# Performance work log

Hardware: AMD Instinct MI355X
Metric: run time of the kernel (lower is better)

Reference implementation:

```python
import jax, jax.numpy as jnp
import numpy as np

N_BEST = 50          # hypotheses per utterance segment
NUM_SEG = 1_000_000  # number of utterance segments
TOTAL = N_BEST * NUM_SEG


def setup_inputs() -> dict:
    key = jax.random.key(0)
    scores = jax.random.normal(key, (TOTAL,), dtype=jnp.float32)
    # per-segment n-best counts; sum(nBestIndex) == len(scores)
    nBestIndex = jnp.full((NUM_SEG,), N_BEST, dtype=jnp.int32)
    return {"scores": scores, "nBestIndex": nBestIndex}


def reference(scores, nBestIndex):
    # Segmented (ragged) softmax: softmax within each contiguous n-best group.
    # Equivalent to the torch loop with log_score=False, fused into one pass.
    num_seg = nBestIndex.shape[0]
    total = scores.shape[0]
    # segment id for each score element
    seg = jnp.repeat(jnp.arange(num_seg, dtype=jnp.int32), nBestIndex,
                     total_repeat_length=total)
    # numerically stable segmented softmax
    seg_max = jax.ops.segment_max(scores, seg, num_segments=num_seg)
    exps = jnp.exp(scores - seg_max[seg])
    seg_sum = jax.ops.segment_sum(exps, seg, num_segments=num_seg)
    return exps / seg_sum[seg]
```

## Files before the change

kernel.cpp:

```cpp
#include <hip/hip_runtime.h>
#include <math.h>


#define GSEG   16
#define SPG    4
#define SBLOCK 256
#define SEGS_B ((SBLOCK / GSEG) * SPG)

__global__ __launch_bounds__(256) void scan_local_kernel(
    const int* __restrict__ counts, int n_seg,
    int* __restrict__ local_scan, int* __restrict__ block_sums) {
    __shared__ int sm[256];
    const int t = threadIdx.x;
    const int g = blockIdx.x * 256 + t;
    const int v = (g < n_seg) ? counts[g] : 0;
    sm[t] = v;
    __syncthreads();
    for (int off = 1; off < 256; off <<= 1) {
        int y = (t >= off) ? sm[t - off] : 0;
        __syncthreads();
        sm[t] += y;
        __syncthreads();
    }
    if (g < n_seg) local_scan[g] = sm[t] - v;
    if (t == 255) block_sums[blockIdx.x] = sm[255];
}

__global__ __launch_bounds__(256) void scan_bsums_kernel(
    int* __restrict__ bsum, int nb) {
    __shared__ int sm[256];
    const int t = threadIdx.x;
    const int per = (nb + 255) >> 8;
    const int beg = t * per;
    const int end = (beg + per < nb) ? beg + per : nb;
    int tot = 0;
    for (int j = beg; j < end; ++j) tot += bsum[j];
    sm[t] = tot;
    __syncthreads();
    for (int off = 1; off < 256; off <<= 1) {
        int y = (t >= off) ? sm[t - off] : 0;
        __syncthreads();
        sm[t] += y;
        __syncthreads();
    }
    int run = sm[t] - tot;
    for (int j = beg; j < end; ++j) {
        int v = bsum[j];
        bsum[j] = run;
        run += v;
    }
}

__global__ __launch_bounds__(SBLOCK) void seg_softmax_kernel(
    const float* __restrict__ scores,
    const int* __restrict__ local_scan, const int* __restrict__ bsum,
    float* __restrict__ out, int n_seg, int total) {
    __shared__ int starts[SEGS_B + 1];

    const int tid  = threadIdx.x;
    const int seg0 = blockIdx.x * SEGS_B;

    if (tid <= SEGS_B) {
        const int s = seg0 + tid;
        starts[tid] = (s < n_seg) ? (local_scan[s] + bsum[s >> 8]) : total;
    }
    __syncthreads();

    const int p   = tid & (GSEG - 1);
    const int grp = tid >> 4;

    int st[SPG], c[SPG];
    #pragma unroll
    for (int q = 0; q < SPG; ++q) {
        const int ls = grp * SPG + q;
        st[q] = starts[ls];
        c[q]  = starts[ls + 1] - st[q];
    }

    bool all_small = true;
    #pragma unroll
    for (int q = 0; q < SPG; ++q) all_small &= (c[q] <= 4 * GSEG);

    if (all_small) {
        float v[SPG][4];
        #pragma unroll
        for (int q = 0; q < SPG; ++q) {
            #pragma unroll
            for (int r = 0; r < 4; ++r) {
                const int idx = p + r * GSEG;
                v[q][r] = (idx < c[q]) ? scores[st[q] + idx] : -INFINITY;
            }
        }

        #pragma unroll
        for (int q = 0; q < SPG; ++q) {
            if (c[q] <= 0) continue;
            float m = fmaxf(fmaxf(v[q][0], v[q][1]), fmaxf(v[q][2], v[q][3]));
            #pragma unroll
            for (int off = 1; off < GSEG; off <<= 1)
                m = fmaxf(m, __shfl_xor(m, off, GSEG));

            const float e0 = __expf(v[q][0] - m);
            const float e1 = __expf(v[q][1] - m);
            const float e2 = __expf(v[q][2] - m);
            const float e3 = __expf(v[q][3] - m);
            float s = (e0 + e1) + (e2 + e3);
            #pragma unroll
            for (int off = 1; off < GSEG; off <<= 1)
                s += __shfl_xor(s, off, GSEG);

            const float inv = __builtin_amdgcn_rcpf(s);
            if (p < c[q])             out[st[q] + p]            = e0 * inv;
            if (p + GSEG < c[q])      out[st[q] + p + GSEG]     = e1 * inv;
            if (p + 2 * GSEG < c[q])  out[st[q] + p + 2 * GSEG] = e2 * inv;
            if (p + 3 * GSEG < c[q])  out[st[q] + p + 3 * GSEG] = e3 * inv;
        }
    } else {
        #pragma unroll
        for (int q = 0; q < SPG; ++q) {
            if (c[q] <= 0) continue;
            float m = -INFINITY;
            for (int j = p; j < c[q]; j += GSEG)
                m = fmaxf(m, scores[st[q] + j]);
            #pragma unroll
            for (int off = 1; off < GSEG; off <<= 1)
                m = fmaxf(m, __shfl_xor(m, off, GSEG));

            float s = 0.0f;
            for (int j = p; j < c[q]; j += GSEG)
                s += __expf(scores[st[q] + j] - m);
            #pragma unroll
            for (int off = 1; off < GSEG; off <<= 1)
                s += __shfl_xor(s, off, GSEG);

            const float inv = __builtin_amdgcn_rcpf(s);
            for (int j = p; j < c[q]; j += GSEG)
                out[st[q] + j] = __expf(scores[st[q] + j] - m) * inv;
        }
    }
}

extern "C" void kernel_launch(void* const* d_in, const int* in_sizes, int n_in,
                              void* d_out, int out_size, void* d_ws, size_t ws_size,
                              hipStream_t stream) {
    const float* scores = (const float*)d_in[0];
    const int*   counts = (const int*)d_in[1];
    float* out = (float*)d_out;
    const int n_seg = in_sizes[1];
    const int total = in_sizes[0];

    int* local_scan = (int*)d_ws;
    const int nblocksA = (n_seg + 255) / 256;
    int* block_sums = local_scan + n_seg;

    scan_local_kernel<<<nblocksA, 256, 0, stream>>>(counts, n_seg, local_scan, block_sums);
    scan_bsums_kernel<<<1, 256, 0, stream>>>(block_sums, nblocksA);

    const int nblocksC = (n_seg + SEGS_B - 1) / SEGS_B;
    seg_softmax_kernel<<<nblocksC, SBLOCK, 0, stream>>>(
        scores, local_scan, block_sums, out, n_seg, total);
}
```

Baseline: 364.7 us.

## Stage each block's contiguous score span in LDS with float4 loads and stores

Each softmax block now copies its whole contiguous score range into shared memory with vectorized float4 global loads, computes the segmented softmax in LDS, and writes the results back with float4 stores. The aim is to replace scattered per-lane scalar global accesses with fully coalesced wide transfers. It adds a 13KB LDS buffer per block, which may limit occupancy, and extra barriers. A fallback path handles spans that are too large or misaligned.

```diff
diff --git a/kernel.cpp b/kernel.cpp
--- a/kernel.cpp
+++ b/kernel.cpp
@@ -6,6 +6,7 @@
 #define SPG    4
 #define SBLOCK 256
 #define SEGS_B ((SBLOCK / GSEG) * SPG)
+#define LDS_FLOATS 3328
 
 __global__ __launch_bounds__(256) void scan_local_kernel(
     const int* __restrict__ counts, int n_seg,
@@ -55,6 +56,7 @@
     const float* __restrict__ scores,
     const int* __restrict__ local_scan, const int* __restrict__ bsum,
     float* __restrict__ out, int n_seg, int total) {
+    __shared__ float sm[LDS_FLOATS];
     __shared__ int starts[SEGS_B + 1];
 
     const int tid  = threadIdx.x;
@@ -64,78 +66,115 @@
         const int s = seg0 + tid;
         starts[tid] = (s < n_seg) ? (local_scan[s] + bsum[s >> 8]) : total;
     }
-    __syncthreads();
-
-    const int p   = tid & (GSEG - 1);
-    const int grp = tid >> 4;
-
-    int st[SPG], c[SPG];
-    #pragma unroll
-    for (int q = 0; q < SPG; ++q) {
-        const int ls = grp * SPG + q;
-        st[q] = starts[ls];
-        c[q]  = starts[ls + 1] - st[q];
-    }
-
-    bool all_small = true;
-    #pragma unroll
-    for (int q = 0; q < SPG; ++q) all_small &= (c[q] <= 4 * GSEG);
-
-    if (all_small) {
-        float v[SPG][4];
+
+    const int base  = local_scan[seg0] + bsum[seg0 >> 8];
+    const int eseg  = seg0 + SEGS_B;
+    const int bend  = (eseg < n_seg) ? (local_scan[eseg] + bsum[eseg >> 8]) : total;
+    const int span  = bend - base;
+
+    if (span <= LDS_FLOATS && (base & 3) == 0) {
+        const float4* __restrict__ src = (const float4*)(scores + base);
+        const int nvec = span >> 2;
+        for (int i = tid; i < nvec; i += SBLOCK)
+            ((float4*)sm)[i] = src[i];
+        for (int i = (nvec << 2) + tid; i < span; i += SBLOCK)
+            sm[i] = scores[base + i];
+        __syncthreads();
+
+        const int p   = tid & (GSEG - 1);
+        const int grp = tid >> 4;
+
+        int st[SPG], c[SPG];
         #pragma unroll
         for (int q = 0; q < SPG; ++q) {
-            #pragma unroll
-            for (int r = 0; r < 4; ++r) {
-                const int idx = p + r * GSEG;
-                v[q][r] = (idx < c[q]) ? scores[st[q] + idx] : -INFINITY;
-            }
+            const int ls = grp * SPG + q;
+            st[q] = starts[ls] - base;
+            c[q]  = starts[ls + 1] - starts[ls];
         }
 
         #pragma unroll
         for (int q = 0; q < SPG; ++q) {
             if (c[q] <= 0) continue;
-            float m = fmaxf(fmaxf(v[q][0], v[q][1]), fmaxf(v[q][2], v[q][3]));
+            if (c[q] <= 4 * GSEG) {
+                float v0 = -INFINITY, v1 = -INFINITY, v2 = -INFINITY, v3 = -INFINITY;
+                const int i0 = p, i1 = p + GSEG, i2 = p + 2 * GSEG, i3 = p + 3 * GSEG;
+                if (i0 < c[q]) v0 = sm[st[q] + i0];
+                if (i1 < c[q]) v1 = sm[st[q] + i1];
+                if (i2 < c[q]) v2 = sm[st[q] + i2];
+                if (i3 < c[q]) v3 = sm[st[q] + i3];
+
+                float m = fmaxf(fmaxf(v0, v1), fmaxf(v2, v3));
+                #pragma unroll
+                for (int off = 1; off < GSEG; off <<= 1)
+                    m = fmaxf(m, __shfl_xor(m, off, GSEG));
+
+                const float e0 = __expf(v0 - m);
+                const float e1 = __expf(v1 - m);
+                const float e2 = __expf(v2 - m);
+                const float e3 = __expf(v3 - m);
+                float s = (e0 + e1) + (e2 + e3);
+                #pragma unroll
+                for (int off = 1; off < GSEG; off <<= 1)
+                    s += __shfl_xor(s, off, GSEG);
+
+                const float inv = __builtin_amdgcn_rcpf(s);
+                if (i0 < c[q]) sm[st[q] + i0] = e0 * inv;
+                if (i1 < c[q]) sm[st[q] + i1] = e1 * inv;
+                if (i2 < c[q]) sm[st[q] + i2] = e2 * inv;
+                if (i3 < c[q]) sm[st[q] + i3] = e3 * inv;
+            } else {
+                float m = -INFINITY;
+                for (int j = p; j < c[q]; j += GSEG)
+                    m = fmaxf(m, sm[st[q] + j]);
+                #pragma unroll
+                for (int off = 1; off < GSEG; off <<= 1)
+                    m = fmaxf(m, __shfl_xor(m, off, GSEG));
+                float s = 0.0f;
+                for (int j = p; j < c[q]; j += GSEG) {
+                    const float e = __expf(sm[st[q] + j] - m);
+                    sm[st[q] + j] = e;
+                    s += e;
+                }
+                #pragma unroll
+                for (int off = 1; off < GSEG; off <<= 1)
+                    s += __shfl_xor(s, off, GSEG);
+                const float inv = __builtin_amdgcn_rcpf(s);
+                for (int j = p; j < c[q]; j += GSEG)
+                    sm[st[q] + j] *= inv;
+            }
+        }
+        __syncthreads();
+
+        float4* __restrict__ dst = (float4*)(out + base);
+        for (int i = tid; i < nvec; i += SBLOCK)
+            dst[i] = ((const float4*)sm)[i];
+        for (int i = (nvec << 2) + tid; i < span; i += SBLOCK)
+            out[base + i] = sm[i];
+    } else {
+        __syncthreads();
+        const int p   = tid & (GSEG - 1);
+        const int grp = tid >> 4;
+        #pragma unroll
+        for (int q = 0; q < SPG; ++q) {
+            const int ls = grp * SPG + q;
+            const int st = starts[ls];
+            const int c  = starts[ls + 1] - st;
+            if (c <= 0) continue;
+            float m = -INFINITY;
+            for (int j = p; j < c; j += GSEG)
+                m = fmaxf(m, scores[st + j]);
             #pragma unroll
             for (int off = 1; off < GSEG; off <<= 1)
                 m = fmaxf(m, __shfl_xor(m, off, GSEG));
-
-            const float e0 = __expf(v[q][0] - m);
-            const float e1 = __expf(v[q][1] - m);
-            const float e2 = __expf(v[q][2] - m);
-            const float e3 = __expf(v[q][3] - m);
-            float s = (e0 + e1) + (e2 + e3);
+            float s = 0.0f;
+            for (int j = p; j < c; j += GSEG)
+                s += __expf(scores[st + j] - m);
             #pragma unroll
             for (int off = 1; off < GSEG; off <<= 1)
                 s += __shfl_xor(s, off, GSEG);
-
             const float inv = __builtin_amdgcn_rcpf(s);
-            if (p < c[q])             out[st[q] + p]            = e0 * inv;
-            if (p + GSEG < c[q])      out[st[q] + p + GSEG]     = e1 * inv;
-            if (p + 2 * GSEG < c[q])  out[st[q] + p + 2 * GSEG] = e2 * inv;
-            if (p + 3 * GSEG < c[q])  out[st[q] + p + 3 * GSEG] = e3 * inv;
-        }
-    } else {
-        #pragma unroll
-        for (int q = 0; q < SPG; ++q) {
-            if (c[q] <= 0) continue;
-            float m = -INFINITY;
-            for (int j = p; j < c[q]; j += GSEG)
-                m = fmaxf(m, scores[st[q] + j]);
-            #pragma unroll
-            for (int off = 1; off < GSEG; off <<= 1)
-                m = fmaxf(m, __shfl_xor(m, off, GSEG));
-
-            float s = 0.0f;
-            for (int j = p; j < c[q]; j += GSEG)
-                s += __expf(scores[st[q] + j] - m);
-            #pragma unroll
-            for (int off = 1; off < GSEG; off <<= 1)
-                s += __shfl_xor(s, off, GSEG);
-
-            const float inv = __builtin_amdgcn_rcpf(s);
-            for (int j = p; j < c[q]; j += GSEG)
-                out[st[q] + j] = __expf(scores[st[q] + j] - m) * inv;
+            for (int j = p; j < c; j += GSEG)
+                out[st + j] = __expf(scores[st + j] - m) * inv;
         }
     }
 }
```

Measured after the change: 351.1 us. 1.04x faster.

## Stage segment spans through LDS with persistent warps and software-prefetched vector loads

Applied to the files above, without the earlier changes.

The softmax kernel becomes a persistent grid-stride kernel in which each wavefront owns a span of 16 segments. It loads the span's contiguous scores with 16-byte vector loads into registers one iteration ahead, stages them through LDS for the per-segment softmax, and writes the span back with coalesced nontemporal vector stores. Segment-start lookups are also prefetched two spans ahead. This aims to replace scattered scalar loads and stores with contiguous vector traffic and to overlap global memory latency with compute, at the cost of 16KB LDS per block, extra register pressure and more complex control flow.

```diff
diff --git a/kernel.cpp b/kernel.cpp
--- a/kernel.cpp
+++ b/kernel.cpp
@@ -2,10 +2,13 @@
 #include <math.h>
 
 
-#define GSEG   16
-#define SPG    4
+typedef float f32x4 __attribute__((ext_vector_type(4)));
+
+#define SEGS_W 16
+#define CAPW   1024
 #define SBLOCK 256
-#define SEGS_B ((SBLOCK / GSEG) * SPG)
+#define WPB    4
+#define GRID_C 2048
 
 __global__ __launch_bounds__(256) void scan_local_kernel(
     const int* __restrict__ counts, int n_seg,
@@ -55,89 +58,179 @@
     const float* __restrict__ scores,
     const int* __restrict__ local_scan, const int* __restrict__ bsum,
     float* __restrict__ out, int n_seg, int total) {
-    __shared__ int starts[SEGS_B + 1];
+
+    __shared__ float buf_all[WPB][CAPW];
 
     const int tid  = threadIdx.x;
-    const int seg0 = blockIdx.x * SEGS_B;
-
-    if (tid <= SEGS_B) {
-        const int s = seg0 + tid;
-        starts[tid] = (s < n_seg) ? (local_scan[s] + bsum[s >> 8]) : total;
-    }
-    __syncthreads();
-
-    const int p   = tid & (GSEG - 1);
-    const int grp = tid >> 4;
-
-    int st[SPG], c[SPG];
-    #pragma unroll
-    for (int q = 0; q < SPG; ++q) {
-        const int ls = grp * SPG + q;
-        st[q] = starts[ls];
-        c[q]  = starts[ls + 1] - st[q];
-    }
-
-    bool all_small = true;
-    #pragma unroll
-    for (int q = 0; q < SPG; ++q) all_small &= (c[q] <= 4 * GSEG);
-
-    if (all_small) {
-        float v[SPG][4];
-        #pragma unroll
-        for (int q = 0; q < SPG; ++q) {
+    const int wv   = tid >> 6;
+    const int lane = tid & 63;
+    float* __restrict__ buf = buf_all[wv];
+
+    const int nspans  = (n_seg + SEGS_W - 1) / SEGS_W;
+    const int wstride = gridDim.x * WPB;
+
+    int t = blockIdx.x * WPB + wv;
+    if (t >= nspans) return;
+
+    const int p = lane & 15;
+    const int g = lane >> 4;
+
+    #define SEG_START(s) (((s) < n_seg) ? (local_scan[(s)] + bsum[(s) >> 8]) : total)
+
+    int tabA = (lane <= SEGS_W) ? SEG_START(t * SEGS_W + lane) : 0;
+    int tn   = t + wstride;
+    int tabB = (tn < nspans && lane <= SEGS_W) ? SEG_START(tn * SEGS_W + lane) : 0;
+
+    int  b0  = __shfl(tabA, 0);
+    int  b1  = __shfl(tabA, SEGS_W);
+    bool fit = ((b1 - b0) <= CAPW) && ((b0 & 3) == 0);
+
+    f32x4 r0, r1, r2, r3;
+    float rt = 0.0f;
+    if (fit) {
+        const f32x4* __restrict__ src = (const f32x4*)(scores + b0);
+        const int nv = (b1 - b0) >> 2, rm = (b1 - b0) & 3;
+        if (lane < nv)        r0 = src[lane];
+        if (lane + 64  < nv)  r1 = src[lane + 64];
+        if (lane + 128 < nv)  r2 = src[lane + 128];
+        if (lane + 192 < nv)  r3 = src[lane + 192];
+        if (lane < rm)        rt = scores[b0 + (nv << 2) + lane];
+    }
+
+    while (true) {
+        const bool haveNext = (tn < nspans);
+        const int  span     = b1 - b0;
+
+        if (fit) {
+            const int nv = span >> 2, rm = span & 3;
+            f32x4* __restrict__ d = (f32x4*)buf;
+            if (lane < nv)        d[lane]       = r0;
+            if (lane + 64  < nv)  d[lane + 64]  = r1;
+            if (lane + 128 < nv)  d[lane + 128] = r2;
+            if (lane + 192 < nv)  d[lane + 192] = r3;
+            if (lane < rm)        buf[(nv << 2) + lane] = rt;
+        }
+
+        int  nb0 = 0, nb1 = 0;
+        bool fitN = false;
+        if (haveNext) {
+            nb0  = __shfl(tabB, 0);
+            nb1  = __shfl(tabB, SEGS_W);
+            fitN = ((nb1 - nb0) <= CAPW) && ((nb0 & 3) == 0);
+            if (fitN) {
+                const f32x4* __restrict__ src = (const f32x4*)(scores + nb0);
+                const int nv2 = (nb1 - nb0) >> 2, rm2 = (nb1 - nb0) & 3;
+                if (lane < nv2)        r0 = src[lane];
+                if (lane + 64  < nv2)  r1 = src[lane + 64];
+                if (lane + 128 < nv2)  r2 = src[lane + 128];
+                if (lane + 192 < nv2)  r3 = src[lane + 192];
+                if (lane < rm2)        rt = scores[nb0 + (nv2 << 2) + lane];
+            }
+        }
+        const int tnn  = tn + wstride;
+        int       tabC = (tnn < nspans && lane <= SEGS_W)
+                         ? SEG_START(tnn * SEGS_W + lane) : 0;
+
+        if (fit) {
             #pragma unroll
-            for (int r = 0; r < 4; ++r) {
-                const int idx = p + r * GSEG;
-                v[q][r] = (idx < c[q]) ? scores[st[q] + idx] : -INFINITY;
+            for (int q = 0; q < 4; ++q) {
+                const int ls = g * 4 + q;
+                const int sA = __shfl(tabA, ls);
+                const int sB = __shfl(tabA, ls + 1);
+                const int c  = sB - sA;
+                const int s0 = sA - b0;
+                if (c <= 0) continue;
+                if (c <= 64) {
+                    const int i0 = p, i1 = p + 16, i2 = p + 32, i3 = p + 48;
+                    float v0 = -INFINITY, v1 = -INFINITY, v2 = -INFINITY, v3 = -INFINITY;
+                    if (i0 < c) v0 = buf[s0 + i0];
+                    if (i1 < c) v1 = buf[s0 + i1];
+                    if (i2 < c) v2 = buf[s0 + i2];
+                    if (i3 < c) v3 = buf[s0 + i3];
+
+                    float m = fmaxf(fmaxf(v0, v1), fmaxf(v2, v3));
+                    #pragma unroll
+                    for (int off = 1; off < 16; off <<= 1)
+                        m = fmaxf(m, __shfl_xor(m, off, 16));
+
+                    const float e0 = __expf(v0 - m);
+                    const float e1 = __expf(v1 - m);
+                    const float e2 = __expf(v2 - m);
+                    const float e3 = __expf(v3 - m);
+                    float s = (e0 + e1) + (e2 + e3);
+                    #pragma unroll
+                    for (int off = 1; off < 16; off <<= 1)
+                        s += __shfl_xor(s, off, 16);
+
+                    const float inv = __builtin_amdgcn_rcpf(s);
+                    if (i0 < c) buf[s0 + i0] = e0 * inv;
+                    if (i1 < c) buf[s0 + i1] = e1 * inv;
+                    if (i2 < c) buf[s0 + i2] = e2 * inv;
+                    if (i3 < c) buf[s0 + i3] = e3 * inv;
+                } else {
+                    float m = -INFINITY;
+                    for (int j = p; j < c; j += 16)
+                        m = fmaxf(m, buf[s0 + j]);
+                    #pragma unroll
+                    for (int off = 1; off < 16; off <<= 1)
+                        m = fmaxf(m, __shfl_xor(m, off, 16));
+                    float s = 0.0f;
+                    for (int j = p; j < c; j += 16) {
+                        const float e = __expf(buf[s0 + j] - m);
+                        buf[s0 + j] = e;
+                        s += e;
+                    }
+                    #pragma unroll
+                    for (int off = 1; off < 16; off <<= 1)
+                        s += __shfl_xor(s, off, 16);
+                    const float inv = __builtin_amdgcn_rcpf(s);
+                    for (int j = p; j < c; j += 16)
+                        buf[s0 + j] *= inv;
+                }
+            }
+
+            const int nv = span >> 2, rm = span & 3;
+            const f32x4* __restrict__ s4 = (const f32x4*)buf;
+            f32x4* __restrict__ dst = (f32x4*)(out + b0);
+            for (int k = lane; k < nv; k += 64) {
+                const f32x4 vv = s4[k];
+                __builtin_nontemporal_store(vv, dst + k);
+            }
+            if (lane < rm)
+                __builtin_nontemporal_store(buf[(nv << 2) + lane],
+                                            out + b0 + (nv << 2) + lane);
+        } else {
+            #pragma unroll
+            for (int q = 0; q < 4; ++q) {
+                const int ls = g * 4 + q;
+                const int sA = __shfl(tabA, ls);
+                const int sB = __shfl(tabA, ls + 1);
+                const int c  = sB - sA;
+                if (c <= 0) continue;
+                float m = -INFINITY;
+                for (int j = p; j < c; j += 16)
+                    m = fmaxf(m, scores[sA + j]);
+                #pragma unroll
+                for (int off = 1; off < 16; off <<= 1)
+                    m = fmaxf(m, __shfl_xor(m, off, 16));
+                float s = 0.0f;
+                for (int j = p; j < c; j += 16)
+                    s += __expf(scores[sA + j] - m);
+                #pragma unroll
+                for (int off = 1; off < 16; off <<= 1)
+                    s += __shfl_xor(s, off, 16);
+                const float inv = __builtin_amdgcn_rcpf(s);
+                for (int j = p; j < c; j += 16)
+                    out[sA + j] = __expf(scores[sA + j] - m) * inv;
             }
         }
 
-        #pragma unroll
-        for (int q = 0; q < SPG; ++q) {
-            if (c[q] <= 0) continue;
-            float m = fmaxf(fmaxf(v[q][0], v[q][1]), fmaxf(v[q][2], v[q][3]));
-            #pragma unroll
-            for (int off = 1; off < GSEG; off <<= 1)
-                m = fmaxf(m, __shfl_xor(m, off, GSEG));
-
-            const float e0 = __expf(v[q][0] - m);
-            const float e1 = __expf(v[q][1] - m);
-            const float e2 = __expf(v[q][2] - m);
-            const float e3 = __expf(v[q][3] - m);
-            float s = (e0 + e1) + (e2 + e3);
-            #pragma unroll
-            for (int off = 1; off < GSEG; off <<= 1)
-                s += __shfl_xor(s, off, GSEG);
-
-            const float inv = __builtin_amdgcn_rcpf(s);
-            if (p < c[q])             out[st[q] + p]            = e0 * inv;
-            if (p + GSEG < c[q])      out[st[q] + p + GSEG]     = e1 * inv;
-            if (p + 2 * GSEG < c[q])  out[st[q] + p + 2 * GSEG] = e2 * inv;
-            if (p + 3 * GSEG < c[q])  out[st[q] + p + 3 * GSEG] = e3 * inv;
-        }
-    } else {
-        #pragma unroll
-        for (int q = 0; q < SPG; ++q) {
-            if (c[q] <= 0) continue;
-            float m = -INFINITY;
-            for (int j = p; j < c[q]; j += GSEG)
-                m = fmaxf(m, scores[st[q] + j]);
-            #pragma unroll
-            for (int off = 1; off < GSEG; off <<= 1)
-                m = fmaxf(m, __shfl_xor(m, off, GSEG));
-
-            float s = 0.0f;
-            for (int j = p; j < c[q]; j += GSEG)
-                s += __expf(scores[st[q] + j] - m);
-            #pragma unroll
-            for (int off = 1; off < GSEG; off <<= 1)
-                s += __shfl_xor(s, off, GSEG);
-
-            const float inv = __builtin_amdgcn_rcpf(s);
-            for (int j = p; j < c[q]; j += GSEG)
-                out[st[q] + j] = __expf(scores[st[q] + j] - m) * inv;
-        }
-    }
+        if (!haveNext) break;
+        t = tn; tn = tnn;
+        tabA = tabB; tabB = tabC;
+        b0 = nb0; b1 = nb1; fit = fitN;
+    }
+    #undef SEG_START
 }
 
 extern "C" void kernel_launch(void* const* d_in, const int* in_sizes, int n_in,
@@ -156,7 +249,9 @@
     scan_local_kernel<<<nblocksA, 256, 0, stream>>>(counts, n_seg, local_scan, block_sums);
     scan_bsums_kernel<<<1, 256, 0, stream>>>(block_sums, nblocksA);
 
-    const int nblocksC = (n_seg + SEGS_B - 1) / SEGS_B;
-    seg_softmax_kernel<<<nblocksC, SBLOCK, 0, stream>>>(
+    const int nspans  = (n_seg + SEGS_W - 1) / SEGS_W;
+    const int nblocksC = (nspans + WPB - 1) / WPB;
+    const int grid     = (nblocksC < GRID_C) ? nblocksC : GRID_C;
+    seg_softmax_kernel<<<grid, SBLOCK, 0, stream>>>(
         scores, local_scan, block_sums, out, n_seg, total);
 }
```

New measurement: 362.0 us. Within noise of the previous version (-0.7%).
